# Kernel tuning notes

Hardware: AMD Instinct MI355X
Metric: run time of the kernel (lower is better)

The kernel has to match this reference:

```python
import jax, jax.numpy as jnp
import numpy as np

BN_EPS = 1e-5


def setup_inputs() -> dict:
    key = jax.random.key(0)
    ks = jax.random.split(key, 16)
    B, C, H, W = 8, 256, 56, 56
    Ci = C // 2  # inter_channels = 128
    s = lambda fan_in: 1.0 / np.sqrt(fan_in)
    return {
        "x": jax.random.normal(ks[0], (B, C, H, W), jnp.float32),
        # 1x1 convs stored as [out, in] matrices
        "g_w": jax.random.normal(ks[1], (Ci, C), jnp.float32) * s(C),
        "g_b": jax.random.normal(ks[2], (Ci,), jnp.float32) * s(C),
        "theta_w": jax.random.normal(ks[3], (Ci, C), jnp.float32) * s(C),
        "theta_b": jax.random.normal(ks[4], (Ci,), jnp.float32) * s(C),
        "phi_w": jax.random.normal(ks[5], (Ci, C), jnp.float32) * s(C),
        "phi_b": jax.random.normal(ks[6], (Ci,), jnp.float32) * s(C),
        # W_f: Conv2d(2*Ci -> 1, k=1)
        "wf_w": jax.random.normal(ks[7], (1, 2 * Ci), jnp.float32) * s(2 * Ci),
        "wf_b": jax.random.normal(ks[8], (1,), jnp.float32) * s(2 * Ci),
        # W_z conv (Ci -> C); source zero-inits; random here for a non-trivial baseline
        "wz_w": jax.random.normal(ks[9], (C, Ci), jnp.float32) * s(Ci),
        "wz_b": jax.random.normal(ks[10], (C,), jnp.float32) * s(Ci),
        # BatchNorm2d (eval mode) params/stats; source zero-inits gamma/beta, randomized here
        "bn_gamma": jax.random.normal(ks[11], (C,), jnp.float32) * 0.1 + 1.0,
        "bn_beta": jax.random.normal(ks[12], (C,), jnp.float32) * 0.1,
        "bn_mean": jax.random.normal(ks[13], (C,), jnp.float32) * 0.1,
        "bn_var": jax.random.uniform(ks[14], (C,), jnp.float32, 0.5, 1.5),
    }


def reference(x, g_w, g_b, theta_w, theta_b, phi_w, phi_b,
              wf_w, wf_b, wz_w, wz_b, bn_gamma, bn_beta, bn_mean, bn_var):
    B, C, H, W = x.shape
    N = H * W
    Ci = g_w.shape[0]
    xf = x.reshape(B, C, N)  # [B, C, N]

    # 1x1 convs over flattened spatial dim
    g_x = jnp.einsum('oc,bcn->bno', g_w, xf) + g_b            # [B, N, Ci]
    theta = jnp.einsum('oc,bcn->bon', theta_w, xf) + theta_b[:, None]  # [B, Ci, N]
    phi = jnp.einsum('oc,bcn->bon', phi_w, xf) + phi_b[:, None]        # [B, Ci, N]

    # W_f over the (repeat+concat) tensor decomposes exactly:
    # f[b,i,j] = relu( w_t . theta[b,:,i] + w_p . phi[b,:,j] + b_f )
    w_t, w_p = wf_w[0, :Ci], wf_w[0, Ci:]
    a = jnp.einsum('c,bcn->bn', w_t, theta)   # [B, N]
    bsc = jnp.einsum('c,bcn->bn', w_p, phi)   # [B, N]
    f = jax.nn.relu(a[:, :, None] + bsc[:, None, :] + wf_b[0])  # [B, N, N]

    y = jnp.matmul(f / N, g_x)                # [B, N, Ci]
    y = y.transpose(0, 2, 1)                  # [B, Ci, N]

    W_y = jnp.einsum('oc,bcn->bon', wz_w, y) + wz_b[:, None]   # [B, C, N]
    inv = bn_gamma / jnp.sqrt(bn_var + BN_EPS)
    W_y = (W_y - bn_mean[:, None]) * inv[:, None] + bn_beta[:, None]

    z = W_y + xf
    return z.reshape(B, C, H, W)
```

## Files before the change

kernel.cpp:

```cpp
#include <hip/hip_runtime.h>
#include <cfloat>
#include <math.h>

#define BATCH 8
#define CH 256
#define CI 128
#define NPIX 3136
#define NCHUNK 98
#define NB 4096
#define BN_EPS 1e-5f

typedef __attribute__((ext_vector_type(8))) short bf16x8;
typedef __attribute__((ext_vector_type(4))) float f32x4;

__device__ __forceinline__ float bf2f(unsigned short u) {
    union { unsigned int i; float f; } x; x.i = ((unsigned int)u) << 16; return x.f;
}
__device__ __forceinline__ unsigned short f2bf(float f) {
    union { float f; unsigned int i; } x; x.f = f;
    unsigned int u = x.i;
    return (unsigned short)((u + 0x7FFFu + ((u >> 16) & 1u)) >> 16);
}

__global__ __launch_bounds__(256) void k_fold(
    const float* __restrict__ wf_w,
    const float* __restrict__ theta_w, const float* __restrict__ theta_b,
    const float* __restrict__ phi_w,   const float* __restrict__ phi_b,
    const float* __restrict__ g_w,     const float* __restrict__ wz_w,
    float* __restrict__ ta_w, float* __restrict__ pb_w, float* __restrict__ biases,
    unsigned short* __restrict__ Bfrag_g, unsigned short* __restrict__ Bfrag_w)
{
    const int bk = blockIdx.x, tid = threadIdx.x;
    if (bk == 0) {
        float ta = 0.f, pb = 0.f;
        for (int c = 0; c < CI; ++c) {
            ta += wf_w[c]      * theta_w[c * CH + tid];
            pb += wf_w[CI + c] * phi_w[c * CH + tid];
        }
        ta_w[tid] = ta;
        pb_w[tid] = pb;
        if (tid == 0) {
            float tb = 0.f, pbb = 0.f;
            for (int c = 0; c < CI; ++c) {
                tb  += wf_w[c]      * theta_b[c];
                pbb += wf_w[CI + c] * phi_b[c];
            }
            biases[0] = tb;
            biases[1] = pbb;
        }
    } else if (bk <= 8) {
        const int base_pair = (bk - 1) * 8;
        for (int e = tid; e < 4096; e += 256) {
            int pp = e >> 9, lane = (e >> 3) & 63, j = e & 7;
            int pair = base_pair + pp;
            int ks = pair >> 3, nt = pair & 7;
            int k = ks * 32 + (lane >> 4) * 8 + j;
            int n = nt * 16 + (lane & 15);
            Bfrag_g[(size_t)pair * 512 + lane * 8 + j] = f2bf(g_w[n * CH + k]);
        }
    } else {
        const int base_pair = (bk - 9) * 8;
        for (int e = tid; e < 4096; e += 256) {
            int pp = e >> 9, lane = (e >> 3) & 63, j = e & 7;
            int pair = base_pair + pp;
            int ks = pair >> 4, nt = pair & 15;
            int k = ks * 32 + (lane >> 4) * 8 + j;
            int n = nt * 16 + (lane & 15);
            Bfrag_w[(size_t)pair * 512 + lane * 8 + j] = f2bf(wz_w[n * CI + k]);
        }
    }
}

__global__ __launch_bounds__(256) void k_gemm(
    const float* __restrict__ x,
    const unsigned short* __restrict__ Bfrag_g,
    const float* __restrict__ g_b,
    const float* __restrict__ ta_w, const float* __restrict__ pb_w,
    const float* __restrict__ biases,
    unsigned short* __restrict__ gxg,
    float* __restrict__ a_out, float* __restrict__ bsc_out)
{
    __shared__ unsigned short gout[64 * 136];

    const int b  = blockIdx.y;
    const int n0 = blockIdx.x * 64;
    const int tid = threadIdx.x;
    const int w = tid >> 6, l = tid & 63, lm = l & 15, lq = l >> 4;
    const int px = n0 + w * 16 + lm;

    const float* xb = x + (size_t)b * CH * NPIX + px;

    bf16x8 af[8];
    float aa = 0.f, pp = 0.f;
#pragma unroll
    for (int ks = 0; ks < 8; ++ks) {
        float v[8];
#pragma unroll
        for (int j = 0; j < 8; ++j) {
            int c = ks * 32 + lq * 8 + j;
            float t = xb[(size_t)c * NPIX];
            v[j] = t;
            aa += ta_w[c] * t;
            pp += pb_w[c] * t;
        }
        union { bf16x8 v8; unsigned short u[8]; } pk;
#pragma unroll
        for (int j = 0; j < 8; ++j) pk.u[j] = f2bf(v[j]);
        af[ks] = pk.v8;
    }

    aa += __shfl_xor(aa, 16); aa += __shfl_xor(aa, 32);
    pp += __shfl_xor(pp, 16); pp += __shfl_xor(pp, 32);
    if (l < 16) {
        a_out[b * NPIX + px]   = aa + biases[0];
        bsc_out[b * NPIX + px] = pp + biases[1];
    }

    f32x4 acc[8];
#pragma unroll
    for (int nt = 0; nt < 8; ++nt) acc[nt] = (f32x4){0.f, 0.f, 0.f, 0.f};

#pragma unroll
    for (int ks = 0; ks < 8; ++ks) {
#pragma unroll
        for (int nt = 0; nt < 8; ++nt) {
            bf16x8 bb = *(const bf16x8*)(Bfrag_g + ((size_t)(ks * 8 + nt) * 64 + l) * 8);
            acc[nt] = __builtin_amdgcn_mfma_f32_16x16x32_bf16(af[ks], bb, acc[nt], 0, 0, 0);
        }
    }

#pragma unroll
    for (int nt = 0; nt < 8; ++nt) {
        int o = nt * 16 + lm;
        float gb = g_b[o];
#pragma unroll
        for (int r = 0; r < 4; ++r) {
            int m = w * 16 + lq * 4 + r;
            gout[m * 136 + o] = f2bf(acc[nt][r] + gb);
        }
    }
    __syncthreads();

    {
        const int n = tid >> 2, ch = tid & 3;
        const uint4* s = (const uint4*)&gout[n * 136 + ch * 32];
        uint4* d = (uint4*)(gxg + ((size_t)(b * NPIX + n0 + n)) * CI + ch * 32);
        d[0] = s[0]; d[1] = s[1]; d[2] = s[2]; d[3] = s[3];
    }
}

__global__ __launch_bounds__(1024) void k_bucketsort(
    const float* __restrict__ bsc,
    float* __restrict__ s_sorted, int* __restrict__ idx_sorted,
    int* __restrict__ bstart, float* __restrict__ params)
{
    __shared__ int hist[NB];
    __shared__ int cnt[NB];
    __shared__ float wmin[16], wmax[16];
    __shared__ int wtot[16], woff[16];
    __shared__ float sh_min, sh_scale;

    const int b = blockIdx.x, tid = threadIdx.x;
    const int lane = tid & 63, wid = tid >> 6;

#pragma unroll
    for (int k = 0; k < 4; ++k) { hist[tid + k * 1024] = 0; cnt[tid + k * 1024] = 0; }

    float v[4];
    float lmin = FLT_MAX, lmax = -FLT_MAX;
#pragma unroll
    for (int k = 0; k < 4; ++k) {
        int i = tid + k * 1024;
        if (i < NPIX) {
            float t = bsc[b * NPIX + i];
            v[k] = t;
            lmin = fminf(lmin, t);
            lmax = fmaxf(lmax, t);
        }
    }
#pragma unroll
    for (int m = 32; m >= 1; m >>= 1) {
        lmin = fminf(lmin, __shfl_xor(lmin, m));
        lmax = fmaxf(lmax, __shfl_xor(lmax, m));
    }
    if (lane == 0) { wmin[wid] = lmin; wmax[wid] = lmax; }
    __syncthreads();

    if (tid < 16) {
        float a = wmin[tid], c = wmax[tid];
#pragma unroll
        for (int m = 8; m >= 1; m >>= 1) {
            a = fminf(a, __shfl_xor(a, m));
            c = fmaxf(c, __shfl_xor(c, m));
        }
        if (tid == 0) {
            float range = c - a;
            float scale = (range > 0.f) ? (float)NB / range : 0.f;
            sh_min = a; sh_scale = scale;
            params[b * 2] = a; params[b * 2 + 1] = scale;
        }
    }
    __syncthreads();

    const float bmin = sh_min, scale = sh_scale;
    int q[4];
#pragma unroll
    for (int k = 0; k < 4; ++k) {
        int i = tid + k * 1024;
        if (i < NPIX) {
            int qq = (int)((v[k] - bmin) * scale);
            qq = (qq < 0) ? 0 : ((qq > NB - 1) ? NB - 1 : qq);
            q[k] = qq;
            atomicAdd(&hist[qq], 1);
        }
    }
    __syncthreads();

    const int base4 = tid * 4;
    int h0 = hist[base4], h1 = hist[base4 + 1], h2 = hist[base4 + 2], h3 = hist[base4 + 3];
    int s = h0 + h1 + h2 + h3;
    int incl = s;
#pragma unroll
    for (int off = 1; off < 64; off <<= 1) {
        int t = __shfl_up(incl, off);
        if (lane >= off) incl += t;
    }
    if (lane == 63) wtot[wid] = incl;
    __syncthreads();
    if (tid < 16) {
        int t = wtot[tid];
        int wi = t;
#pragma unroll
        for (int off = 1; off < 16; off <<= 1) {
            int u = __shfl_up(wi, off);
            if (tid >= off) wi += u;
        }
        woff[tid] = wi - t;
    }
    __syncthreads();
    int excl = woff[wid] + (incl - s);
    hist[base4]     = excl;
    hist[base4 + 1] = excl + h0;
    hist[base4 + 2] = excl + h0 + h1;
    hist[base4 + 3] = excl + h0 + h1 + h2;
    __syncthreads();

#pragma unroll
    for (int k = 0; k < 4; ++k) {
        int i = tid + k * 1024;
        bstart[b * (NB + 1) + i] = hist[i];
    }
    if (tid == 0) bstart[b * (NB + 1) + NB] = NPIX;

#pragma unroll
    for (int k = 0; k < 4; ++k) {
        int i = tid + k * 1024;
        if (i < NPIX) {
            int pos = hist[q[k]] + atomicAdd(&cnt[q[k]], 1);
            s_sorted[b * NPIX + pos]   = v[k];
            idx_sorted[b * NPIX + pos] = i;
        }
    }
}

__global__ __launch_bounds__(64) void k_csum(
    const unsigned short* __restrict__ gxg,
    const float* __restrict__ s_sorted, const int* __restrict__ idx_sorted,
    float* __restrict__ CS1, float* __restrict__ CS2)
{
    const int b = blockIdx.y, c = blockIdx.x, t = threadIdx.x;
    const int base = b * NPIX + c * 32;

    int   my_i = idx_sorted[base + (t & 31)];
    float my_v = s_sorted[base + (t & 31)];

    float a1x = 0.f, a1y = 0.f, a2x = 0.f, a2y = 0.f;
#pragma unroll 8
    for (int rr = 0; rr < 32; ++rr) {
        int   row = __shfl(my_i, rr);
        float sv  = __shfl(my_v, rr);
        unsigned int u = *(const unsigned int*)(gxg + ((size_t)(b * NPIX + row)) * CI + 2 * t);
        float v0 = bf2f((unsigned short)(u & 0xffffu));
        float v1 = bf2f((unsigned short)(u >> 16));
        a1x += v0;      a1y += v1;
        a2x += sv * v0; a2y += sv * v1;
    }
    float2* p1 = (float2*)&CS1[(b * 100 + c) * CI];
    float2* p2 = (float2*)&CS2[(b * 100 + c) * CI];
    p1[t] = make_float2(a1x, a1y);
    p2[t] = make_float2(a2x, a2y);
}

__global__ __launch_bounds__(1024) void k_suffix(
    float* __restrict__ CS1, float* __restrict__ CS2)
{
    __shared__ float buf[NCHUNK * CI];
    __shared__ float tot[8][CI];
    const int b = blockIdx.x, tid = threadIdx.x;
    float* __restrict__ CS = blockIdx.y ? CS2 : CS1;

    for (int i = tid; i < NCHUNK * CI; i += 1024) buf[i] = CS[b * 100 * CI + i];
    __syncthreads();

    const int seg = tid >> 7, o = tid & 127;
    const int c0 = seg * 13;
    const int c1 = (seg == 7) ? NCHUNK : c0 + 13;
    {
        float acc = 0.f;
        for (int c = c1 - 1; c >= c0; --c) {
            acc += buf[c * CI + o];
            buf[c * CI + o] = acc;
        }
        tot[seg][o] = acc;
    }
    __syncthreads();
    {
        float off = 0.f;
#pragma unroll
        for (int s2 = 7; s2 >= 1; --s2) if (s2 > seg) off += tot[s2][o];
        if (off != 0.f || seg < 7) {
            for (int c = c0; c < c1; ++c) buf[c * CI + o] += off;
        }
    }
    __syncthreads();
    for (int i = tid; i < NCHUNK * CI; i += 1024) CS[b * 100 * CI + i] = buf[i];
    if (tid < CI) {
        CS[(b * 100 + 98) * CI + tid] = 0.f;
        CS[(b * 100 + 99) * CI + tid] = 0.f;
    }
}

__global__ __launch_bounds__(256) void k_final(
    const float* __restrict__ x,
    const float* __restrict__ a_arr, const float* __restrict__ wf_b,
    const float* __restrict__ CS1, const float* __restrict__ CS2,
    const int* __restrict__ bstart, const float* __restrict__ params,
    const unsigned short* __restrict__ Bfrag_w,
    const float* __restrict__ wz_b,
    const float* __restrict__ bn_g, const float* __restrict__ bn_b,
    const float* __restrict__ bn_m, const float* __restrict__ bn_v,
    float* __restrict__ out)
{
    __shared__ unsigned short ys[64 * 136];
    __shared__ int   rs[64];
    __shared__ float ts[64];

    const int b = blockIdx.y;
    const int n0 = blockIdx.x * 64;
    const int tid = threadIdx.x;

    if (tid < 64) {
        float t = a_arr[b * NPIX + n0 + tid] + wf_b[0];
        float bmin = params[b * 2], scale = params[b * 2 + 1];
        float fq = (-t - bmin) * scale;
        int kb = (int)(fq + 0.5f);
        kb = (kb < 0) ? 0 : ((kb > NB) ? NB : kb);
        int r = bstart[b * (NB + 1) + kb];
        int cstar = (r + 16) >> 5;
        cstar = (cstar > 98) ? 98 : cstar;
        rs[tid] = cstar;
        ts[tid] = t;
    }
    __syncthreads();

    const int o = tid & 127;
    const int h = tid >> 7;
    const float invN = 1.0f / (float)NPIX;

#pragma unroll 4
    for (int i = 0; i < 32; ++i) {
        int n = h * 32 + i;
        int cb = (b * 100 + rs[n]) * CI + o;
        float S1 = CS1[cb], S2 = CS2[cb];
        ys[n * 136 + o] = f2bf((ts[n] * S1 + S2) * invN);
    }
    __syncthreads();

    const int w = tid >> 6, l = tid & 63, lm = l & 15, lq = l >> 4;

    float invv[4], biasv[4];
#pragma unroll
    for (int ni = 0; ni < 4; ++ni) {
        int cc = w * 64 + ni * 16 + lm;
        float iv = bn_g[cc] * rsqrtf(bn_v[cc] + BN_EPS);
        invv[ni] = iv;
        biasv[ni] = (wz_b[cc] - bn_m[cc]) * iv + bn_b[cc];
    }

    f32x4 acc[4][4];
#pragma unroll
    for (int mi = 0; mi < 4; ++mi)
#pragma unroll
        for (int ni = 0; ni < 4; ++ni) acc[mi][ni] = (f32x4){0.f, 0.f, 0.f, 0.f};

#pragma unroll
    for (int ks = 0; ks < 4; ++ks) {
        bf16x8 af[4];
#pragma unroll
        for (int mi = 0; mi < 4; ++mi)
            af[mi] = *(const bf16x8*)&ys[(mi * 16 + lm) * 136 + ks * 32 + lq * 8];
#pragma unroll
        for (int ni = 0; ni < 4; ++ni) {
            bf16x8 bb = *(const bf16x8*)(Bfrag_w + ((size_t)(ks * 16 + w * 4 + ni) * 64 + l) * 8);
#pragma unroll
            for (int mi = 0; mi < 4; ++mi)
                acc[mi][ni] = __builtin_amdgcn_mfma_f32_16x16x32_bf16(af[mi], bb, acc[mi][ni], 0, 0, 0);
        }
    }

#pragma unroll
    for (int mi = 0; mi < 4; ++mi)
#pragma unroll
        for (int ni = 0; ni < 4; ++ni) {
            int cc = w * 64 + ni * 16 + lm;
            int m  = mi * 16 + lq * 4;
            size_t base = ((size_t)b * CH + cc) * NPIX + n0 + m;
            const float4 xv = *(const float4*)(x + base);
            float4 ov;
            ov.x = acc[mi][ni][0] * invv[ni] + biasv[ni] + xv.x;
            ov.y = acc[mi][ni][1] * invv[ni] + biasv[ni] + xv.y;
            ov.z = acc[mi][ni][2] * invv[ni] + biasv[ni] + xv.z;
            ov.w = acc[mi][ni][3] * invv[ni] + biasv[ni] + xv.w;
            *(float4*)(out + base) = ov;
        }
}

extern "C" void kernel_launch(void* const* d_in, const int* in_sizes, int n_in,
                              void* d_out, int out_size, void* d_ws, size_t ws_size,
                              hipStream_t stream)
{
    const float* x       = (const float*)d_in[0];
    const float* g_w     = (const float*)d_in[1];
    const float* g_b     = (const float*)d_in[2];
    const float* theta_w = (const float*)d_in[3];
    const float* theta_b = (const float*)d_in[4];
    const float* phi_w   = (const float*)d_in[5];
    const float* phi_b   = (const float*)d_in[6];
    const float* wf_w    = (const float*)d_in[7];
    const float* wf_b    = (const float*)d_in[8];
    const float* wz_w    = (const float*)d_in[9];
    const float* wz_b    = (const float*)d_in[10];
    const float* bn_g    = (const float*)d_in[11];
    const float* bn_b    = (const float*)d_in[12];
    const float* bn_m    = (const float*)d_in[13];
    const float* bn_v    = (const float*)d_in[14];

    float* ws = (float*)d_ws;
    float* ta_w   = ws;
    float* pb_w   = ws + 256;
    float* biases = ws + 512;
    float* params = ws + 516;
    float* a_arr  = ws + 532;
    float* bsc      = a_arr + BATCH * NPIX;
    float* s_sorted = bsc + BATCH * NPIX;
    int*   idx_sorted = (int*)(s_sorted + BATCH * NPIX);
    int*   bstart   = idx_sorted + BATCH * NPIX;
    float* CS1    = (float*)(bstart + BATCH * (NB + 1));
    float* CS2    = CS1 + BATCH * 100 * CI;
    unsigned short* Bfrag_g = (unsigned short*)(CS2 + BATCH * 100 * CI);
    unsigned short* Bfrag_w = Bfrag_g + 32768;
    unsigned short* gxg = Bfrag_w + 32768;

    k_fold<<<17, 256, 0, stream>>>(wf_w, theta_w, theta_b, phi_w, phi_b,
                                   g_w, wz_w, ta_w, pb_w, biases,
                                   Bfrag_g, Bfrag_w);

    k_gemm<<<dim3(49, BATCH), 256, 0, stream>>>(
        x, Bfrag_g, g_b, ta_w, pb_w, biases, gxg, a_arr, bsc);

    k_bucketsort<<<BATCH, 1024, 0, stream>>>(bsc, s_sorted, idx_sorted,
                                             bstart, params);

    k_csum<<<dim3(NCHUNK, BATCH), 64, 0, stream>>>(
        gxg, s_sorted, idx_sorted, CS1, CS2);

    k_suffix<<<dim3(BATCH, 2), 1024, 0, stream>>>(CS1, CS2);

    k_final<<<dim3(49, BATCH), 256, 0, stream>>>(
        x, a_arr, wf_b, CS1, CS2, bstart, params, Bfrag_w,
        wz_b, bn_g, bn_b, bn_m, bn_v, (float*)d_out);
}
```

Baseline: 153.7 us.

## Fuse bucket sort, chunk sums and suffix scan into one kernel

Merges the bucket-sort, per-chunk gather-sum and suffix-scan kernels into a single per-batch kernel of 1024 threads. The chunk sums live in shared memory, which also holds the sort histogram, and the scan runs twice: once for the plain sums and once for the score-weighted sums, kept in registers between passes. This removes two kernel launches and the global round trip of the partial sums. The trade-off is that the gather of all gx rows now runs on only 8 workgroups instead of 784 small ones, so that step gets far less parallelism.

```diff
diff --git a/kernel.cpp b/kernel.cpp
--- a/kernel.cpp
+++ b/kernel.cpp
@@ -149,16 +149,21 @@
     }
 }
 
-__global__ __launch_bounds__(1024) void k_bucketsort(
+__global__ __launch_bounds__(1024) void k_sortsum(
     const float* __restrict__ bsc,
+    const unsigned short* __restrict__ gxg,
     float* __restrict__ s_sorted, int* __restrict__ idx_sorted,
-    int* __restrict__ bstart, float* __restrict__ params)
+    int* __restrict__ bstart, float* __restrict__ params,
+    float* __restrict__ CS1, float* __restrict__ CS2)
 {
-    __shared__ int hist[NB];
-    __shared__ int cnt[NB];
+    __shared__ float CS[NCHUNK * CI];
+    __shared__ float tot[8][CI];
     __shared__ float wmin[16], wmax[16];
     __shared__ int wtot[16], woff[16];
     __shared__ float sh_min, sh_scale;
+
+    int* hist = (int*)CS;
+    int* cnt  = hist + NB;
 
     const int b = blockIdx.x, tid = threadIdx.x;
     const int lane = tid & 63, wid = tid >> 6;
@@ -261,45 +266,32 @@
             idx_sorted[b * NPIX + pos] = i;
         }
     }
-}
-
-__global__ __launch_bounds__(64) void k_csum(
-    const unsigned short* __restrict__ gxg,
-    const float* __restrict__ s_sorted, const int* __restrict__ idx_sorted,
-    float* __restrict__ CS1, float* __restrict__ CS2)
-{
-    const int b = blockIdx.y, c = blockIdx.x, t = threadIdx.x;
-    const int base = b * NPIX + c * 32;
-
-    int   my_i = idx_sorted[base + (t & 31)];
-    float my_v = s_sorted[base + (t & 31)];
-
-    float a1x = 0.f, a1y = 0.f, a2x = 0.f, a2y = 0.f;
+    __syncthreads();
+
+    float2 a2save[7];
+    int nown = 0;
+    for (int c = wid; c < NCHUNK; c += 16) {
+        const int base = b * NPIX + c * 32;
+        int   my_i = 0; float my_v = 0.f;
+        if (lane < 32) {
+            my_i = idx_sorted[base + lane];
+            my_v = s_sorted[base + lane];
+        }
+        float a1x = 0.f, a1y = 0.f, a2x = 0.f, a2y = 0.f;
 #pragma unroll 8
-    for (int rr = 0; rr < 32; ++rr) {
-        int   row = __shfl(my_i, rr);
-        float sv  = __shfl(my_v, rr);
-        unsigned int u = *(const unsigned int*)(gxg + ((size_t)(b * NPIX + row)) * CI + 2 * t);
-        float v0 = bf2f((unsigned short)(u & 0xffffu));
-        float v1 = bf2f((unsigned short)(u >> 16));
-        a1x += v0;      a1y += v1;
-        a2x += sv * v0; a2y += sv * v1;
-    }
-    float2* p1 = (float2*)&CS1[(b * 100 + c) * CI];
-    float2* p2 = (float2*)&CS2[(b * 100 + c) * CI];
-    p1[t] = make_float2(a1x, a1y);
-    p2[t] = make_float2(a2x, a2y);
-}
-
-__global__ __launch_bounds__(1024) void k_suffix(
-    float* __restrict__ CS1, float* __restrict__ CS2)
-{
-    __shared__ float buf[NCHUNK * CI];
-    __shared__ float tot[8][CI];
-    const int b = blockIdx.x, tid = threadIdx.x;
-    float* __restrict__ CS = blockIdx.y ? CS2 : CS1;
-
-    for (int i = tid; i < NCHUNK * CI; i += 1024) buf[i] = CS[b * 100 * CI + i];
+        for (int rr = 0; rr < 32; ++rr) {
+            int   row = __shfl(my_i, rr);
+            float sv  = __shfl(my_v, rr);
+            unsigned int u = *(const unsigned int*)(gxg + ((size_t)(b * NPIX + row)) * CI + 2 * lane);
+            float v0 = bf2f((unsigned short)(u & 0xffffu));
+            float v1 = bf2f((unsigned short)(u >> 16));
+            a1x += v0;      a1y += v1;
+            a2x += sv * v0; a2y += sv * v1;
+        }
+        CS[c * CI + 2 * lane]     = a1x;
+        CS[c * CI + 2 * lane + 1] = a1y;
+        a2save[nown++] = make_float2(a2x, a2y);
+    }
     __syncthreads();
 
     const int seg = tid >> 7, o = tid & 127;
@@ -308,8 +300,8 @@
     {
         float acc = 0.f;
         for (int c = c1 - 1; c >= c0; --c) {
-            acc += buf[c * CI + o];
-            buf[c * CI + o] = acc;
+            acc += CS[c * CI + o];
+            CS[c * CI + o] = acc;
         }
         tot[seg][o] = acc;
     }
@@ -319,14 +311,46 @@
 #pragma unroll
         for (int s2 = 7; s2 >= 1; --s2) if (s2 > seg) off += tot[s2][o];
         if (off != 0.f || seg < 7) {
-            for (int c = c0; c < c1; ++c) buf[c * CI + o] += off;
-        }
-    }
-    __syncthreads();
-    for (int i = tid; i < NCHUNK * CI; i += 1024) CS[b * 100 * CI + i] = buf[i];
+            for (int c = c0; c < c1; ++c) CS[c * CI + o] += off;
+        }
+    }
+    __syncthreads();
+    for (int i = tid; i < NCHUNK * CI; i += 1024) CS1[b * 100 * CI + i] = CS[i];
     if (tid < CI) {
-        CS[(b * 100 + 98) * CI + tid] = 0.f;
-        CS[(b * 100 + 99) * CI + tid] = 0.f;
+        CS1[(b * 100 + 98) * CI + tid] = 0.f;
+        CS1[(b * 100 + 99) * CI + tid] = 0.f;
+    }
+    __syncthreads();
+
+    nown = 0;
+    for (int c = wid; c < NCHUNK; c += 16) {
+        CS[c * CI + 2 * lane]     = a2save[nown].x;
+        CS[c * CI + 2 * lane + 1] = a2save[nown].y;
+        ++nown;
+    }
+    __syncthreads();
+    {
+        float acc = 0.f;
+        for (int c = c1 - 1; c >= c0; --c) {
+            acc += CS[c * CI + o];
+            CS[c * CI + o] = acc;
+        }
+        tot[seg][o] = acc;
+    }
+    __syncthreads();
+    {
+        float off = 0.f;
+#pragma unroll
+        for (int s2 = 7; s2 >= 1; --s2) if (s2 > seg) off += tot[s2][o];
+        if (off != 0.f || seg < 7) {
+            for (int c = c0; c < c1; ++c) CS[c * CI + o] += off;
+        }
+    }
+    __syncthreads();
+    for (int i = tid; i < NCHUNK * CI; i += 1024) CS2[b * 100 * CI + i] = CS[i];
+    if (tid < CI) {
+        CS2[(b * 100 + 98) * CI + tid] = 0.f;
+        CS2[(b * 100 + 99) * CI + tid] = 0.f;
     }
 }
 
@@ -468,13 +492,8 @@
     k_gemm<<<dim3(49, BATCH), 256, 0, stream>>>(
         x, Bfrag_g, g_b, ta_w, pb_w, biases, gxg, a_arr, bsc);
 
-    k_bucketsort<<<BATCH, 1024, 0, stream>>>(bsc, s_sorted, idx_sorted,
-                                             bstart, params);
-
-    k_csum<<<dim3(NCHUNK, BATCH), 64, 0, stream>>>(
-        gxg, s_sorted, idx_sorted, CS1, CS2);
-
-    k_suffix<<<dim3(BATCH, 2), 1024, 0, stream>>>(CS1, CS2);
+    k_sortsum<<<BATCH, 1024, 0, stream>>>(
+        bsc, gxg, s_sorted, idx_sorted, bstart, params, CS1, CS2);
 
     k_final<<<dim3(49, BATCH), 256, 0, stream>>>(
         x, a_arr, wf_b, CS1, CS2, bstart, params, Bfrag_w,
```

Measured after the change: 167.9 us. 1.09x slower.
